# Optimization experiments

Measured on AMD Instinct MI355X. Metric: run time of the kernel, lower is better.

## Reference

```python
import jax, jax.numpy as jnp
import numpy as np

B, H, W, C = 16, 56, 56, 512
WS, NH = 7, 16
HD = C // NH
HID = 4 * C
N = WS * WS
NW = (H // WS) * (W // WS)
SCALE = HD ** -0.5
EPS = 1e-5


def _layernorm(x, g, b):
    mu = jnp.mean(x, axis=-1, keepdims=True)
    var = jnp.mean(jnp.square(x - mu), axis=-1, keepdims=True)
    return (x - mu) * jax.lax.rsqrt(var + EPS) * g + b


def _win_part(t):
    # (B,H,W,C) -> (B*nw, NH, N, HD)
    t = t.reshape(B, H // WS, WS, W // WS, WS, C).transpose(0, 1, 3, 2, 4, 5)
    return t.reshape(B * NW, N, NH, HD).transpose(0, 2, 1, 3)


def setup_inputs() -> dict:
    key = jax.random.key(0)
    ks = jax.random.split(key, 20)
    p = lambda k, shp: (jax.random.normal(k, shp, dtype=jnp.float32) * 0.02)
    return {
        "x": jax.random.normal(ks[0], (B, H * W, C), dtype=jnp.float32),
        "Wq": p(ks[1], (C, C)), "bq": jnp.zeros((C,), jnp.float32),
        "Wk": p(ks[2], (C, C)), "bk": jnp.zeros((C,), jnp.float32),
        "Wv": p(ks[3], (C, C)), "bv": jnp.zeros((C,), jnp.float32),
        "Wp": p(ks[4], (C, C)), "bp": jnp.zeros((C,), jnp.float32),
        "rel_bias": p(ks[5], (1, NH, N, N)),
        "g1": jnp.ones((C,), jnp.float32), "b1": jnp.zeros((C,), jnp.float32),
        "g2": jnp.ones((C,), jnp.float32), "b2": jnp.zeros((C,), jnp.float32),
        "W1": p(ks[6], (C, HID)), "bfc1": jnp.zeros((HID,), jnp.float32),
        "W2": p(ks[7], (HID, C)), "bfc2": jnp.zeros((C,), jnp.float32),
    }


def reference(x, Wq, bq, Wk, bk, Wv, bv, Wp, bp, rel_bias,
              g1, b1, g2, b2, W1, bfc1, W2, bfc2):
    shortcut = x                                   # (B, L, C)
    h = _layernorm(x, g1, b1).reshape(B, H, W, C)
    q = _win_part(h @ Wq + bq)                     # (B*nw, NH, N, HD)
    k = _win_part(h @ Wk + bk)
    v = _win_part(h @ Wv + bv)
    attn = jnp.einsum("whnd,whmd->whnm", q * SCALE, k) + rel_bias
    attn = jax.nn.softmax(attn, axis=-1)
    out = jnp.einsum("whnm,whmd->whnd", attn, v)   # (B*nw, NH, N, HD)
    out = out.transpose(0, 2, 1, 3).reshape(B * NW, N, C)
    out = out @ Wp + bp
    # window reverse -> (B, L, C)
    out = out.reshape(B, H // WS, W // WS, WS, WS, C)
    out = out.transpose(0, 1, 3, 2, 4, 5).reshape(B, H * W, C)
    x = shortcut + out
    h2 = _layernorm(x, g2, b2)
    h2 = jax.nn.gelu(h2 @ W1 + bfc1, approximate=False) @ W2 + bfc2
    return x + h2
```

## Files before the change

kernel.cpp:

```cpp
#include <hip/hip_runtime.h>

typedef unsigned short u16;
typedef unsigned int   u32;

using short8  = __attribute__((ext_vector_type(8))) short;
using floatx4 = __attribute__((ext_vector_type(4))) float;

#define Bb   16
#define Hh   56
#define Ww   56
#define Cc   512
#define NHh  16
#define HDd  32
#define HIDh 2048
#define Ll   (Hh*Ww)
#define Mm   (Bb*Ll)
#define SCALE 0.17677669529663687f
#define CSTR 136

__device__ __forceinline__ u16 f2bf(float f) {
  union { float f; u32 u; } v; v.f = f;
  u32 r = (v.u + 0x7fffu + ((v.u >> 16) & 1u)) >> 16;
  return (u16)r;
}
__device__ __forceinline__ float bf2f(u16 u) {
  union { u32 u; float f; } v; v.u = ((u32)u) << 16; return v.f;
}
__device__ __forceinline__ float bf2f_lo(u32 u) {
  union { u32 u; float f; } v; v.u = u << 16; return v.f;
}
__device__ __forceinline__ float bf2f_hi(u32 u) {
  union { u32 u; float f; } v; v.u = u & 0xffff0000u; return v.f;
}
__device__ __forceinline__ float gelu_f(float x) {
  const float z  = x * 0.70710678118654752f;
  const float az = fabsf(z);
  const float t  = __builtin_amdgcn_rcpf(fmaf(0.3275911f, az, 1.f));
  float p = fmaf(1.061405429f, t, -1.453152027f);
  p = fmaf(p, t, 1.421413741f);
  p = fmaf(p, t, -0.284496736f);
  p = fmaf(p, t, 0.254829592f);
  const float e = p * t * __expf(-z * z);
  float erfz = 1.f - e;
  erfz = copysignf(erfz, z);
  return 0.5f * x * (1.f + erfz);
}
__device__ __forceinline__ void gld_lds16(const u16* g, u16* l) {
  __builtin_amdgcn_global_load_lds(
      (__attribute__((address_space(1))) void*)(void*)g,
      (__attribute__((address_space(3))) void*)(void*)l,
      16, 0, 0);
}

__global__ void wcvt_k(const float* __restrict__ W, u16* __restrict__ Wt,
                       int K, int N) {
  int idx = blockIdx.x * 256 + threadIdx.x;
  int n = idx / K;
  int k = idx - n * K;
  Wt[idx] = f2bf(W[(size_t)k * N + n]);
}

__global__ void bcat_k(const float* __restrict__ a, const float* __restrict__ b,
                       const float* __restrict__ c, float* __restrict__ o) {
  int i = blockIdx.x * 256 + threadIdx.x;
  float v = (i < 512) ? a[i] : (i < 1024) ? b[i - 512] : c[i - 1024];
  o[i] = v;
}

__global__ __launch_bounds__(256)
void ln_k(const float* __restrict__ x, const float* __restrict__ g,
          const float* __restrict__ b, u16* __restrict__ out) {
  const int row  = blockIdx.x * 4 + (threadIdx.x >> 6);
  const int lane = threadIdx.x & 63;
  const float* xr = x + (size_t)row * Cc + lane * 8;
  float4 v0 = *(const float4*)xr;
  float4 v1 = *(const float4*)(xr + 4);
  float s  = v0.x+v0.y+v0.z+v0.w + v1.x+v1.y+v1.z+v1.w;
  float s2 = v0.x*v0.x+v0.y*v0.y+v0.z*v0.z+v0.w*v0.w
           + v1.x*v1.x+v1.y*v1.y+v1.z*v1.z+v1.w*v1.w;
  #pragma unroll
  for (int off = 32; off >= 1; off >>= 1) {
    s  += __shfl_xor(s,  off);
    s2 += __shfl_xor(s2, off);
  }
  float mu  = s  * (1.f/512.f);
  float var = s2 * (1.f/512.f) - mu*mu;
  float rs  = rsqrtf(var + 1e-5f);
  float4 ga = *(const float4*)(g + lane*8);
  float4 gb = *(const float4*)(g + lane*8 + 4);
  float4 ba = *(const float4*)(b + lane*8);
  float4 bb = *(const float4*)(b + lane*8 + 4);
  float o0 = (v0.x-mu)*rs*ga.x + ba.x;
  float o1 = (v0.y-mu)*rs*ga.y + ba.y;
  float o2 = (v0.z-mu)*rs*ga.z + ba.z;
  float o3 = (v0.w-mu)*rs*ga.w + ba.w;
  float o4 = (v1.x-mu)*rs*gb.x + bb.x;
  float o5 = (v1.y-mu)*rs*gb.y + bb.y;
  float o6 = (v1.z-mu)*rs*gb.z + bb.z;
  float o7 = (v1.w-mu)*rs*gb.w + bb.w;
  u32 w0 = (u32)f2bf(o0) | ((u32)f2bf(o1) << 16);
  u32 w1 = (u32)f2bf(o2) | ((u32)f2bf(o3) << 16);
  u32 w2 = (u32)f2bf(o4) | ((u32)f2bf(o5) << 16);
  u32 w3 = (u32)f2bf(o6) | ((u32)f2bf(o7) << 16);
  *(uint4*)(out + (size_t)row * Cc + lane * 8) = make_uint4(w0, w1, w2, w3);
}

__global__ __launch_bounds__(256)
void ln_bf_k(const u16* __restrict__ x, const float* __restrict__ g,
             const float* __restrict__ b, u16* __restrict__ out) {
  const int row  = blockIdx.x * 4 + (threadIdx.x >> 6);
  const int lane = threadIdx.x & 63;
  uint4 xv = *(const uint4*)(x + (size_t)row * Cc + lane * 8);
  float v[8];
  v[0]=bf2f_lo(xv.x); v[1]=bf2f_hi(xv.x); v[2]=bf2f_lo(xv.y); v[3]=bf2f_hi(xv.y);
  v[4]=bf2f_lo(xv.z); v[5]=bf2f_hi(xv.z); v[6]=bf2f_lo(xv.w); v[7]=bf2f_hi(xv.w);
  float s = 0.f, s2 = 0.f;
  #pragma unroll
  for (int i = 0; i < 8; i++) { s += v[i]; s2 += v[i]*v[i]; }
  #pragma unroll
  for (int off = 32; off >= 1; off >>= 1) {
    s  += __shfl_xor(s,  off);
    s2 += __shfl_xor(s2, off);
  }
  float mu  = s  * (1.f/512.f);
  float var = s2 * (1.f/512.f) - mu*mu;
  float rs  = rsqrtf(var + 1e-5f);
  float4 ga = *(const float4*)(g + lane*8);
  float4 gb = *(const float4*)(g + lane*8 + 4);
  float4 ba = *(const float4*)(b + lane*8);
  float4 bb = *(const float4*)(b + lane*8 + 4);
  float o[8];
  o[0]=(v[0]-mu)*rs*ga.x+ba.x; o[1]=(v[1]-mu)*rs*ga.y+ba.y;
  o[2]=(v[2]-mu)*rs*ga.z+ba.z; o[3]=(v[3]-mu)*rs*ga.w+ba.w;
  o[4]=(v[4]-mu)*rs*gb.x+bb.x; o[5]=(v[5]-mu)*rs*gb.y+bb.y;
  o[6]=(v[6]-mu)*rs*gb.z+bb.z; o[7]=(v[7]-mu)*rs*gb.w+bb.w;
  u32 w0 = (u32)f2bf(o[0]) | ((u32)f2bf(o[1]) << 16);
  u32 w1 = (u32)f2bf(o[2]) | ((u32)f2bf(o[3]) << 16);
  u32 w2 = (u32)f2bf(o[4]) | ((u32)f2bf(o[5]) << 16);
  u32 w3 = (u32)f2bf(o[6]) | ((u32)f2bf(o[7]) << 16);
  *(uint4*)(out + (size_t)row * Cc + lane * 8) = make_uint4(w0, w1, w2, w3);
}

template<int MODE>
__global__ __launch_bounds__(256, 4)
void gemm_bt(const u16* __restrict__ A, const u16* __restrict__ Bt,
             const float* __restrict__ bias, const void* __restrict__ res,
             void* __restrict__ outp, int M, int N, int K, int nbn) {
  (void)M;
  __shared__ __align__(16) u16 smem[128 * CSTR];

  const int b   = blockIdx.x;
  const int xcd = b & 7;
  const int s   = b >> 3;
  const int mt  = (s / nbn) * 8 + xcd;
  const int nt  = s - (s / nbn) * nbn;
  const int m0  = mt * 128;
  const int n0  = nt * 128;

  const int tid  = threadIdx.x;
  const int lane = tid & 63;
  const int wave = tid >> 6;
  const int wm = (wave >> 1) * 64;
  const int wn = (wave & 1) * 64;
  const int quad = lane >> 4;
  const int l16  = lane & 15;

  floatx4 acc[4][4];
  #pragma unroll
  for (int i = 0; i < 4; i++)
    #pragma unroll
    for (int j = 0; j < 4; j++) acc[i][j] = (floatx4)0.f;

  const int r0  = tid >> 2;
  const int cc0 = (((tid & 3) ^ ((r0 >> 1) & 3)) * 8);
  const u16* Ag = A  + (size_t)m0 * K;
  const u16* Bg = Bt + (size_t)n0 * K;

  const int fswz = (l16 >> 1) & 3;
  const int aoff = (quad ^ fswz) * 8;

#define STG(kk, bufo) do {                                                        \
    gld_lds16(Ag + (size_t)r0        * K + (kk) + cc0, &smem[(bufo) + wave * 512]);        \
    gld_lds16(Ag + (size_t)(r0 + 64) * K + (kk) + cc0, &smem[(bufo) + 2048 + wave * 512]); \
    gld_lds16(Bg + (size_t)r0        * K + (kk) + cc0, &smem[(bufo) + 4096 + wave * 512]); \
    gld_lds16(Bg + (size_t)(r0 + 64) * K + (kk) + cc0, &smem[(bufo) + 6144 + wave * 512]); \
  } while (0)

  STG(0, 0);
  asm volatile("s_waitcnt vmcnt(0)" ::: "memory");
  __builtin_amdgcn_s_barrier();

  for (int k0 = 0; k0 < K; k0 += 32) {
    const int bufo = ((k0 >> 5) & 1) * 8192;
    if (k0 + 32 < K) STG(k0 + 32, bufo ^ 8192);
    const u16* As = &smem[bufo];
    const u16* Bs = &smem[bufo + 4096];
    short8 af[4], bf[4];
    #pragma unroll
    for (int mi = 0; mi < 4; mi++)
      af[mi] = *(const short8*)&As[(wm + mi*16 + l16) * 32 + aoff];
    #pragma unroll
    for (int ni = 0; ni < 4; ni++)
      bf[ni] = *(const short8*)&Bs[(wn + ni*16 + l16) * 32 + aoff];
    #pragma unroll
    for (int mi = 0; mi < 4; mi++)
      #pragma unroll
      for (int ni = 0; ni < 4; ni++)
        acc[mi][ni] = __builtin_amdgcn_mfma_f32_16x16x32_bf16(
            af[mi], bf[ni], acc[mi][ni], 0, 0, 0);
    asm volatile("s_waitcnt vmcnt(0)" ::: "memory");
    __builtin_amdgcn_s_barrier();
  }
#undef STG

  if (MODE == 3) {
    const int mrow = m0 + wm + quad * 4;
    const int ncol = n0 + wn + l16;
    #pragma unroll
    for (int ni = 0; ni < 4; ni++) {
      const int n = ncol + ni * 16;
      const float bv = bias[n];
      #pragma unroll
      for (int mi = 0; mi < 4; mi++)
        #pragma unroll
        for (int r = 0; r < 4; r++) {
          const size_t idx = (size_t)(mrow + mi * 16 + r) * N + n;
          ((float*)outp)[idx] = acc[mi][ni][r] + bv + bf2f(((const u16*)res)[idx]);
        }
    }
  } else {
    #pragma unroll
    for (int ni = 0; ni < 4; ni++) {
      const int col = wn + ni * 16 + l16;
      const float bv = bias[n0 + col];
      #pragma unroll
      for (int mi = 0; mi < 4; mi++)
        #pragma unroll
        for (int r = 0; r < 4; r++) {
          float v = acc[mi][ni][r] + bv;
          if (MODE == 1) v = gelu_f(v);
          smem[(wm + mi * 16 + quad * 4 + r) * CSTR + col] = f2bf(v);
        }
    }
    __syncthreads();
    const int trow = tid >> 4;
    const int tcol = (tid & 15) * 8;
    #pragma unroll
    for (int it = 0; it < 8; it++) {
      const int row = it * 16 + trow;
      uint4 w = *(const uint4*)&smem[row * CSTR + tcol];
      const size_t gi = (size_t)(m0 + row) * N + n0 + tcol;
      if (MODE == 2) {
        const float* rp = (const float*)res + gi;
        float4 ra = *(const float4*)rp;
        float4 rb = *(const float4*)(rp + 4);
        u32 w0 = (u32)f2bf(bf2f_lo(w.x) + ra.x) | ((u32)f2bf(bf2f_hi(w.x) + ra.y) << 16);
        u32 w1 = (u32)f2bf(bf2f_lo(w.y) + ra.z) | ((u32)f2bf(bf2f_hi(w.y) + ra.w) << 16);
        u32 w2 = (u32)f2bf(bf2f_lo(w.z) + rb.x) | ((u32)f2bf(bf2f_hi(w.z) + rb.y) << 16);
        u32 w3 = (u32)f2bf(bf2f_lo(w.w) + rb.z) | ((u32)f2bf(bf2f_hi(w.w) + rb.w) << 16);
        *(uint4*)((u16*)outp + gi) = make_uint4(w0, w1, w2, w3);
      } else {
        *(uint4*)((u16*)outp + gi) = w;
      }
    }
  }
}

__global__ __launch_bounds__(64)
void attn_k(const u16* __restrict__ QKV, const float* __restrict__ rel,
            u16* __restrict__ O) {
  const int win  = blockIdx.x;
  const int head = blockIdx.y;
  const int b    = win >> 6;
  const int wh   = (win >> 3) & 7;
  const int ww   = win & 7;
  const int lane = threadIdx.x;

  __shared__ float Ks[49][36];
  __shared__ float Vs[49][36];

  const bool active = lane < 49;
  size_t rowq = 0, rowo = 0;
  float q[32];
  if (active) {
    const int i = lane / 7, j = lane - 7 * (lane / 7);
    const int l = (wh * 7 + i) * Ww + ww * 7 + j;
    const size_t gr = (size_t)(b * Ll + l);
    rowq = gr * 1536 + head * HDd;
    rowo = gr * 512  + head * HDd;
    const uint4* qp = (const uint4*)(QKV + rowq);
    const uint4* kp = (const uint4*)(QKV + rowq + 512);
    const uint4* vp = (const uint4*)(QKV + rowq + 1024);
    #pragma unroll
    for (int c = 0; c < 4; c++) {
      uint4 qv = qp[c], kv = kp[c], vv = vp[c];
      q[c*8+0] = bf2f_lo(qv.x) * SCALE; q[c*8+1] = bf2f_hi(qv.x) * SCALE;
      q[c*8+2] = bf2f_lo(qv.y) * SCALE; q[c*8+3] = bf2f_hi(qv.y) * SCALE;
      q[c*8+4] = bf2f_lo(qv.z) * SCALE; q[c*8+5] = bf2f_hi(qv.z) * SCALE;
      q[c*8+6] = bf2f_lo(qv.w) * SCALE; q[c*8+7] = bf2f_hi(qv.w) * SCALE;
      *(float4*)&Ks[lane][c*8]   = make_float4(bf2f_lo(kv.x), bf2f_hi(kv.x),
                                               bf2f_lo(kv.y), bf2f_hi(kv.y));
      *(float4*)&Ks[lane][c*8+4] = make_float4(bf2f_lo(kv.z), bf2f_hi(kv.z),
                                               bf2f_lo(kv.w), bf2f_hi(kv.w));
      *(float4*)&Vs[lane][c*8]   = make_float4(bf2f_lo(vv.x), bf2f_hi(vv.x),
                                               bf2f_lo(vv.y), bf2f_hi(vv.y));
      *(float4*)&Vs[lane][c*8+4] = make_float4(bf2f_lo(vv.z), bf2f_hi(vv.z),
                                               bf2f_lo(vv.w), bf2f_hi(vv.w));
    }
  }
  __syncthreads();
  if (!active) return;

  const float* rb = rel + ((size_t)head * 49 + lane) * 49;
  float s[49];
  float mx = -1e30f;
  #pragma unroll
  for (int m = 0; m < 49; m++) {
    float d = 0.f;
    #pragma unroll
    for (int c = 0; c < 8; c++) {
      float4 kk = *(const float4*)&Ks[m][c*4];
      d += q[c*4+0]*kk.x + q[c*4+1]*kk.y + q[c*4+2]*kk.z + q[c*4+3]*kk.w;
    }
    d += rb[m];
    s[m] = d;
    mx = fmaxf(mx, d);
  }
  float sum = 0.f;
  #pragma unroll
  for (int m = 0; m < 49; m++) { float e = __expf(s[m] - mx); s[m] = e; sum += e; }
  const float inv = 1.f / sum;

  float acc[32];
  #pragma unroll
  for (int d = 0; d < 32; d++) acc[d] = 0.f;
  #pragma unroll
  for (int m = 0; m < 49; m++) {
    const float p = s[m];
    #pragma unroll
    for (int c = 0; c < 8; c++) {
      float4 vv = *(const float4*)&Vs[m][c*4];
      acc[c*4+0] += p*vv.x; acc[c*4+1] += p*vv.y;
      acc[c*4+2] += p*vv.z; acc[c*4+3] += p*vv.w;
    }
  }
  uint4* op = (uint4*)(O + rowo);
  #pragma unroll
  for (int c = 0; c < 4; c++) {
    u32 w0 = (u32)f2bf(acc[c*8+0]*inv) | ((u32)f2bf(acc[c*8+1]*inv) << 16);
    u32 w1 = (u32)f2bf(acc[c*8+2]*inv) | ((u32)f2bf(acc[c*8+3]*inv) << 16);
    u32 w2 = (u32)f2bf(acc[c*8+4]*inv) | ((u32)f2bf(acc[c*8+5]*inv) << 16);
    u32 w3 = (u32)f2bf(acc[c*8+6]*inv) | ((u32)f2bf(acc[c*8+7]*inv) << 16);
    op[c] = make_uint4(w0, w1, w2, w3);
  }
}

extern "C" void kernel_launch(void* const* d_in, const int* in_sizes, int n_in,
                              void* d_out, int out_size, void* d_ws, size_t ws_size,
                              hipStream_t stream) {
  (void)in_sizes; (void)n_in; (void)out_size; (void)ws_size;
  const float* x    = (const float*)d_in[0];
  const float* Wq   = (const float*)d_in[1];
  const float* bq   = (const float*)d_in[2];
  const float* Wk   = (const float*)d_in[3];
  const float* bk   = (const float*)d_in[4];
  const float* Wv   = (const float*)d_in[5];
  const float* bv   = (const float*)d_in[6];
  const float* Wp   = (const float*)d_in[7];
  const float* bp   = (const float*)d_in[8];
  const float* rel  = (const float*)d_in[9];
  const float* g1   = (const float*)d_in[10];
  const float* b1   = (const float*)d_in[11];
  const float* g2   = (const float*)d_in[12];
  const float* b2   = (const float*)d_in[13];
  const float* W1   = (const float*)d_in[14];
  const float* bfc1 = (const float*)d_in[15];
  const float* W2   = (const float*)d_in[16];
  const float* bfc2 = (const float*)d_in[17];
  float* out = (float*)d_out;

  u16* wQKV = (u16*)d_ws;
  u16* wWp  = wQKV + (size_t)1536*512;
  u16* wW1  = wWp  + (size_t)512*512;
  u16* wW2  = wW1  + (size_t)2048*512;
  float* bqkv = (float*)(wW2 + (size_t)512*2048);
  u16* hbuf = (u16*)(bqkv + 1536);
  u16* QKVb = hbuf + (size_t)Mm * Cc;
  u16* Obuf = QKVb + (size_t)Mm * 1536;
  u16* x2bf = Obuf + (size_t)Mm * Cc;
  u16* hid  = QKVb;
  u16* h2   = hbuf;

  wcvt_k<<<(512*512)/256,  256, 0, stream>>>(Wq, wQKV,              512, 512);
  wcvt_k<<<(512*512)/256,  256, 0, stream>>>(Wk, wQKV + 512*512,    512, 512);
  wcvt_k<<<(512*512)/256,  256, 0, stream>>>(Wv, wQKV + 2*512*512,  512, 512);
  wcvt_k<<<(512*512)/256,  256, 0, stream>>>(Wp, wWp, 512, 512);
  wcvt_k<<<(512*2048)/256, 256, 0, stream>>>(W1, wW1, 512, 2048);
  wcvt_k<<<(512*2048)/256, 256, 0, stream>>>(W2, wW2, 2048, 512);
  bcat_k<<<6, 256, 0, stream>>>(bq, bk, bv, bqkv);

  ln_k<<<Mm/4, 256, 0, stream>>>(x, g1, b1, hbuf);

  gemm_bt<0><<<392*12, 256, 0, stream>>>(hbuf, wQKV, bqkv, nullptr, QKVb,
                                         Mm, 1536, 512, 12);

  attn_k<<<dim3(1024, 16), 64, 0, stream>>>(QKVb, rel, Obuf);

  gemm_bt<2><<<392*4, 256, 0, stream>>>(Obuf, wWp, bp, x, x2bf,
                                        Mm, 512, 512, 4);

  ln_bf_k<<<Mm/4, 256, 0, stream>>>(x2bf, g2, b2, h2);

  gemm_bt<1><<<392*16, 256, 0, stream>>>(h2, wW1, bfc1, nullptr, hid,
                                         Mm, 2048, 512, 16);
  gemm_bt<3><<<392*4, 256, 0, stream>>>(hid, wW2, bfc2, x2bf, out,
                                        Mm, 512, 2048, 4);
}
```

Baseline: 910.6 us.

## Rewrite window attention with bf16 MFMA for QK^T and PV

The scalar-FP32 window attention kernel is replaced with one that uses 16x16x32 bf16 MFMA for both QK^T and P·V. Each 256-thread block handles four heads of one window, one wave per head. A new prep kernel lays out the relative-position bias in MFMA accumulator fragment order, with -inf padding for masked columns, so it can be added directly to the scores. Softmax runs on fragments using cross-lane shuffles, and P and V^T are staged through LDS in bf16. This trades FP32 precision in P for bf16 and adds LDS staging plus padding waste, since 49 rows are padded to 64.

```diff
diff --git a/kernel.cpp b/kernel.cpp
--- a/kernel.cpp
+++ b/kernel.cpp
@@ -17,6 +17,7 @@
 #define Mm   (Bb*Ll)
 #define SCALE 0.17677669529663687f
 #define CSTR 136
+#define PSTR 72
 
 __device__ __forceinline__ u16 f2bf(float f) {
   union { float f; u32 u; } v; v.f = f;
@@ -65,6 +66,22 @@
   int i = blockIdx.x * 256 + threadIdx.x;
   float v = (i < 512) ? a[i] : (i < 1024) ? b[i - 512] : c[i - 1024];
   o[i] = v;
+}
+
+__global__ void relprep_k(const float* __restrict__ rel, float* __restrict__ relL) {
+  int idx  = blockIdx.x * 256 + threadIdx.x;
+  int reg  = idx & 3;
+  int lane = (idx >> 2) & 63;
+  int frag = (idx >> 8) & 15;
+  int h    = idx >> 12;
+  int mi = frag >> 2, nj = frag & 3;
+  int row = mi * 16 + (lane >> 4) * 4 + reg;
+  int col = nj * 16 + (lane & 15);
+  float v;
+  if (col >= 49)      v = -1e30f;
+  else if (row >= 49) v = 0.f;
+  else                v = rel[((size_t)h * 49 + row) * 49 + col];
+  relL[idx] = v;
 }
 
 __global__ __launch_bounds__(256)
@@ -266,92 +283,169 @@
   }
 }
 
-__global__ __launch_bounds__(64)
-void attn_k(const u16* __restrict__ QKV, const float* __restrict__ rel,
+__global__ __launch_bounds__(256, 3)
+void attn_k(const u16* __restrict__ QKV, const float* __restrict__ relL,
             u16* __restrict__ O) {
-  const int win  = blockIdx.x;
-  const int head = blockIdx.y;
+  __shared__ __align__(16) u16 Vt[4][32][PSTR];
+  __shared__ __align__(16) u16 Pl[4][49 * PSTR];
+
+  const int tid  = threadIdx.x;
+  const int wave = tid >> 6;
+  const int lane = tid & 63;
+  const int quad = lane >> 4;
+  const int l16  = lane & 15;
+
+  const int win  = blockIdx.x >> 2;
+  const int head = ((blockIdx.x & 3) << 2) + wave;
   const int b    = win >> 6;
   const int wh   = (win >> 3) & 7;
   const int ww   = win & 7;
-  const int lane = threadIdx.x;
-
-  __shared__ float Ks[49][36];
-  __shared__ float Vs[49][36];
-
-  const bool active = lane < 49;
-  size_t rowq = 0, rowo = 0;
-  float q[32];
-  if (active) {
-    const int i = lane / 7, j = lane - 7 * (lane / 7);
-    const int l = (wh * 7 + i) * Ww + ww * 7 + j;
-    const size_t gr = (size_t)(b * Ll + l);
-    rowq = gr * 1536 + head * HDd;
-    rowo = gr * 512  + head * HDd;
-    const uint4* qp = (const uint4*)(QKV + rowq);
-    const uint4* kp = (const uint4*)(QKV + rowq + 512);
-    const uint4* vp = (const uint4*)(QKV + rowq + 1024);
-    #pragma unroll
-    for (int c = 0; c < 4; c++) {
-      uint4 qv = qp[c], kv = kp[c], vv = vp[c];
-      q[c*8+0] = bf2f_lo(qv.x) * SCALE; q[c*8+1] = bf2f_hi(qv.x) * SCALE;
-      q[c*8+2] = bf2f_lo(qv.y) * SCALE; q[c*8+3] = bf2f_hi(qv.y) * SCALE;
-      q[c*8+4] = bf2f_lo(qv.z) * SCALE; q[c*8+5] = bf2f_hi(qv.z) * SCALE;
-      q[c*8+6] = bf2f_lo(qv.w) * SCALE; q[c*8+7] = bf2f_hi(qv.w) * SCALE;
-      *(float4*)&Ks[lane][c*8]   = make_float4(bf2f_lo(kv.x), bf2f_hi(kv.x),
-                                               bf2f_lo(kv.y), bf2f_hi(kv.y));
-      *(float4*)&Ks[lane][c*8+4] = make_float4(bf2f_lo(kv.z), bf2f_hi(kv.z),
-                                               bf2f_lo(kv.w), bf2f_hi(kv.w));
-      *(float4*)&Vs[lane][c*8]   = make_float4(bf2f_lo(vv.x), bf2f_hi(vv.x),
-                                               bf2f_lo(vv.y), bf2f_hi(vv.y));
-      *(float4*)&Vs[lane][c*8+4] = make_float4(bf2f_lo(vv.z), bf2f_hi(vv.z),
-                                               bf2f_lo(vv.w), bf2f_hi(vv.w));
-    }
-  }
-  __syncthreads();
-  if (!active) return;
-
-  const float* rb = rel + ((size_t)head * 49 + lane) * 49;
-  float s[49];
-  float mx = -1e30f;
-  #pragma unroll
-  for (int m = 0; m < 49; m++) {
-    float d = 0.f;
-    #pragma unroll
-    for (int c = 0; c < 8; c++) {
-      float4 kk = *(const float4*)&Ks[m][c*4];
-      d += q[c*4+0]*kk.x + q[c*4+1]*kk.y + q[c*4+2]*kk.z + q[c*4+3]*kk.w;
-    }
-    d += rb[m];
-    s[m] = d;
-    mx = fmaxf(mx, d);
-  }
-  float sum = 0.f;
-  #pragma unroll
-  for (int m = 0; m < 49; m++) { float e = __expf(s[m] - mx); s[m] = e; sum += e; }
-  const float inv = 1.f / sum;
-
-  float acc[32];
-  #pragma unroll
-  for (int d = 0; d < 32; d++) acc[d] = 0.f;
-  #pragma unroll
-  for (int m = 0; m < 49; m++) {
-    const float p = s[m];
-    #pragma unroll
-    for (int c = 0; c < 8; c++) {
-      float4 vv = *(const float4*)&Vs[m][c*4];
-      acc[c*4+0] += p*vv.x; acc[c*4+1] += p*vv.y;
-      acc[c*4+2] += p*vv.z; acc[c*4+3] += p*vv.w;
-    }
-  }
-  uint4* op = (uint4*)(O + rowo);
-  #pragma unroll
-  for (int c = 0; c < 4; c++) {
-    u32 w0 = (u32)f2bf(acc[c*8+0]*inv) | ((u32)f2bf(acc[c*8+1]*inv) << 16);
-    u32 w1 = (u32)f2bf(acc[c*8+2]*inv) | ((u32)f2bf(acc[c*8+3]*inv) << 16);
-    u32 w2 = (u32)f2bf(acc[c*8+4]*inv) | ((u32)f2bf(acc[c*8+5]*inv) << 16);
-    u32 w3 = (u32)f2bf(acc[c*8+6]*inv) | ((u32)f2bf(acc[c*8+7]*inv) << 16);
-    op[c] = make_uint4(w0, w1, w2, w3);
+  const int base_l = b * Ll + (wh * 7) * Ww + ww * 7;
+
+  u32 vw[16];
+  #pragma unroll
+  for (int i = 0; i < 16; i++) vw[i] = 0;
+  const int lc = lane < 49 ? lane : 48;
+  const size_t grl = (size_t)base_l + (lc / 7) * 56 + (lc % 7);
+  if (lane < 49) {
+    const uint4* vp = (const uint4*)(QKV + grl * 1536 + 1024 + head * HDd);
+    uint4 a0 = vp[0], a1 = vp[1], a2 = vp[2], a3 = vp[3];
+    vw[0]=a0.x;  vw[1]=a0.y;  vw[2]=a0.z;  vw[3]=a0.w;
+    vw[4]=a1.x;  vw[5]=a1.y;  vw[6]=a1.z;  vw[7]=a1.w;
+    vw[8]=a2.x;  vw[9]=a2.y;  vw[10]=a2.z; vw[11]=a2.w;
+    vw[12]=a3.x; vw[13]=a3.y; vw[14]=a3.z; vw[15]=a3.w;
+  }
+  {
+    u16* vtb = &Vt[wave][0][lane];
+    #pragma unroll
+    for (int c = 0; c < 32; c++)
+      vtb[c * PSTR] = (u16)(vw[c >> 1] >> ((c & 1) << 4));
+  }
+
+  size_t gr16[4];
+  #pragma unroll
+  for (int t = 0; t < 4; t++) {
+    int r = t * 16 + l16; if (r > 48) r = 48;
+    gr16[t] = (size_t)base_l + (r / 7) * 56 + (r % 7);
+  }
+  short8 qf[4], kf[4];
+  #pragma unroll
+  for (int t = 0; t < 4; t++) {
+    qf[t] = *(const short8*)(QKV + gr16[t] * 1536 + head * HDd + quad * 8);
+    kf[t] = *(const short8*)(QKV + gr16[t] * 1536 + 512 + head * HDd + quad * 8);
+  }
+
+  floatx4 acc[4][4];
+  #pragma unroll
+  for (int mi = 0; mi < 4; mi++)
+    #pragma unroll
+    for (int nj = 0; nj < 4; nj++) acc[mi][nj] = (floatx4)0.f;
+  #pragma unroll
+  for (int mi = 0; mi < 4; mi++)
+    #pragma unroll
+    for (int nj = 0; nj < 4; nj++)
+      acc[mi][nj] = __builtin_amdgcn_mfma_f32_16x16x32_bf16(
+          qf[mi], kf[nj], acc[mi][nj], 0, 0, 0);
+
+  const float* rlb = relL + ((size_t)head << 12) + lane * 4;
+  #pragma unroll
+  for (int mi = 0; mi < 4; mi++)
+    #pragma unroll
+    for (int nj = 0; nj < 4; nj++) {
+      float4 rl = *(const float4*)(rlb + ((mi * 4 + nj) << 8));
+      acc[mi][nj][0] = fmaf(acc[mi][nj][0], SCALE, rl.x);
+      acc[mi][nj][1] = fmaf(acc[mi][nj][1], SCALE, rl.y);
+      acc[mi][nj][2] = fmaf(acc[mi][nj][2], SCALE, rl.z);
+      acc[mi][nj][3] = fmaf(acc[mi][nj][3], SCALE, rl.w);
+    }
+
+  float sums[4][4];
+  #pragma unroll
+  for (int mi = 0; mi < 4; mi++)
+    #pragma unroll
+    for (int r = 0; r < 4; r++) {
+      float mx = fmaxf(fmaxf(acc[mi][0][r], acc[mi][1][r]),
+                       fmaxf(acc[mi][2][r], acc[mi][3][r]));
+      #pragma unroll
+      for (int off = 8; off >= 1; off >>= 1)
+        mx = fmaxf(mx, __shfl_xor(mx, off));
+      float sm = 0.f;
+      #pragma unroll
+      for (int nj = 0; nj < 4; nj++) {
+        float e = __expf(acc[mi][nj][r] - mx);
+        acc[mi][nj][r] = e;
+        sm += e;
+      }
+      #pragma unroll
+      for (int off = 8; off >= 1; off >>= 1)
+        sm += __shfl_xor(sm, off);
+      sums[mi][r] = sm;
+    }
+
+  u16* Pw = Pl[wave];
+  {
+    u16* pb = Pw + (quad * 4) * PSTR + l16;
+    #pragma unroll
+    for (int mi = 0; mi < 3; mi++)
+      #pragma unroll
+      for (int r = 0; r < 4; r++)
+        #pragma unroll
+        for (int nj = 0; nj < 4; nj++)
+          pb[(mi * 16 + r) * PSTR + nj * 16] = f2bf(acc[mi][nj][r]);
+    if (quad == 0) {
+      #pragma unroll
+      for (int nj = 0; nj < 4; nj++)
+        pb[48 * PSTR + nj * 16] = f2bf(acc[3][nj][0]);
+    }
+  }
+  asm volatile("s_waitcnt lgkmcnt(0)" ::: "memory");
+
+  floatx4 pv[4][2];
+  #pragma unroll
+  for (int mi = 0; mi < 4; mi++)
+    #pragma unroll
+    for (int nj = 0; nj < 2; nj++) pv[mi][nj] = (floatx4)0.f;
+  #pragma unroll
+  for (int ks = 0; ks < 2; ks++) {
+    short8 pf[4], vf[2];
+    #pragma unroll
+    for (int mi = 0; mi < 4; mi++) {
+      const int pr = (mi < 3) ? (mi * 16 + l16) : 48;
+      pf[mi] = *(const short8*)&Pw[pr * PSTR + ks * 32 + quad * 8];
+    }
+    #pragma unroll
+    for (int nj = 0; nj < 2; nj++)
+      vf[nj] = *(const short8*)&Vt[wave][nj * 16 + l16][ks * 32 + quad * 8];
+    #pragma unroll
+    for (int mi = 0; mi < 4; mi++)
+      #pragma unroll
+      for (int nj = 0; nj < 2; nj++)
+        pv[mi][nj] = __builtin_amdgcn_mfma_f32_16x16x32_bf16(
+            pf[mi], vf[nj], pv[mi][nj], 0, 0, 0);
+  }
+
+  asm volatile("s_waitcnt lgkmcnt(0)" ::: "memory");
+  {
+    u16* ob = Pw + (quad * 4) * PSTR + l16;
+    #pragma unroll
+    for (int mi = 0; mi < 3; mi++)
+      #pragma unroll
+      for (int r = 0; r < 4; r++) {
+        const float inv = __builtin_amdgcn_rcpf(sums[mi][r]);
+        ob[(mi * 16 + r) * PSTR +  0] = f2bf(pv[mi][0][r] * inv);
+        ob[(mi * 16 + r) * PSTR + 16] = f2bf(pv[mi][1][r] * inv);
+      }
+    if (quad == 0) {
+      const float inv = __builtin_amdgcn_rcpf(sums[3][0]);
+      ob[48 * PSTR +  0] = f2bf(pv[3][0][0] * inv);
+      ob[48 * PSTR + 16] = f2bf(pv[3][1][0] * inv);
+    }
+  }
+  asm volatile("s_waitcnt lgkmcnt(0)" ::: "memory");
+  if (lane < 49) {
+    const uint4* orow = (const uint4*)&Pw[lane * PSTR];
+    uint4* op = (uint4*)(O + grl * 512 + head * HDd);
+    op[0] = orow[0]; op[1] = orow[1]; op[2] = orow[2]; op[3] = orow[3];
   }
 }
 
@@ -384,7 +478,8 @@
   u16* wW1  = wWp  + (size_t)512*512;
   u16* wW2  = wW1  + (size_t)2048*512;
   float* bqkv = (float*)(wW2 + (size_t)512*2048);
-  u16* hbuf = (u16*)(bqkv + 1536);
+  float* relL = bqkv + 1536;
+  u16* hbuf = (u16*)(relL + 65536);
   u16* QKVb = hbuf + (size_t)Mm * Cc;
   u16* Obuf = QKVb + (size_t)Mm * 1536;
   u16* x2bf = Obuf + (size_t)Mm * Cc;
@@ -398,13 +493,14 @@
   wcvt_k<<<(512*2048)/256, 256, 0, stream>>>(W1, wW1, 512, 2048);
   wcvt_k<<<(512*2048)/256, 256, 0, stream>>>(W2, wW2, 2048, 512);
   bcat_k<<<6, 256, 0, stream>>>(bq, bk, bv, bqkv);
+  relprep_k<<<65536/256, 256, 0, stream>>>(rel, relL);
 
   ln_k<<<Mm/4, 256, 0, stream>>>(x, g1, b1, hbuf);
 
   gemm_bt<0><<<392*12, 256, 0, stream>>>(hbuf, wQKV, bqkv, nullptr, QKVb,
                                          Mm, 1536, 512, 12);
 
-  attn_k<<<dim3(1024, 16), 64, 0, stream>>>(QKVb, rel, Obuf);
+  attn_k<<<4096, 256, 0, stream>>>(QKVb, relL, Obuf);
 
   gemm_bt<2><<<392*4, 256, 0, stream>>>(Obuf, wWp, bp, x, x2bf,
                                         Mm, 512, 512, 4);
```

Result: faster. 799.1 us (-12.2%).
